# Kernel tuning notes

Hardware: AMD Instinct MI355X
Metric: run time of the kernel (lower is better)

Reference implementation:

```python
import jax, jax.numpy as jnp
import numpy as np
from jax import lax

B, L, D = 2, 1024, 1024
EXPAND, N, K = 2, 16, 4          # expand, d_state, d_conv
DI = EXPAND * D                  # d_inner = 2048
R = (D + 15) // 16               # dt_rank = 64
EPS = 1e-5


def setup_inputs() -> dict:
    key = jax.random.key(0)
    ks = jax.random.split(key, 8)
    x = jax.random.normal(ks[0], (B, L, D), dtype=jnp.float32)
    ln_w = jnp.ones((D,), jnp.float32)
    ln_b = jnp.zeros((D,), jnp.float32)
    W_in = jax.random.normal(ks[1], (D, 2 * DI), jnp.float32) * (1.0 / np.sqrt(D))
    conv_w = jax.random.normal(ks[2], (DI, K), jnp.float32) * 0.2
    conv_b = jnp.zeros((DI,), jnp.float32)
    W_x = jax.random.normal(ks[3], (DI, R + 2 * N), jnp.float32) * (1.0 / np.sqrt(DI))
    W_dt = jax.random.normal(ks[4], (R, DI), jnp.float32) * (1.0 / np.sqrt(R))
    b_dt = jnp.full((DI,), -4.0, jnp.float32)  # softplus(-4) ~ 0.018 dt init
    A_log = jnp.log(jnp.broadcast_to(jnp.arange(1, N + 1, dtype=jnp.float32), (DI, N)))
    D_param = jnp.ones((DI,), jnp.float32)
    W_out = jax.random.normal(ks[5], (DI, D), jnp.float32) * (1.0 / np.sqrt(DI))
    return {"x": x, "ln_w": ln_w, "ln_b": ln_b, "W_in": W_in, "conv_w": conv_w,
            "conv_b": conv_b, "W_x": W_x, "W_dt": W_dt, "b_dt": b_dt,
            "A_log": A_log, "D_param": D_param, "W_out": W_out}


def _mamba_block(x, ln_w, ln_b, W_in, conv_w, conv_b, W_x, W_dt, b_dt, A_log, D_param, W_out):
    # pre-LayerNorm
    mu = jnp.mean(x, axis=-1, keepdims=True)
    xc = x - mu
    var = jnp.mean(xc * xc, axis=-1, keepdims=True)
    h = xc * lax.rsqrt(var + EPS) * ln_w + ln_b          # [B,L,D]

    xz = h @ W_in                                        # [B,L,2*DI]
    xi, z = xz[..., :DI], xz[..., DI:]

    # depthwise causal conv1d, kernel K, left pad K-1
    xp = jnp.pad(xi, ((0, 0), (K - 1, 0), (0, 0)))
    conv = conv_b
    for k in range(K):
        conv = conv + xp[:, k:k + L, :] * conv_w[:, k]
    u = jax.nn.silu(conv)                                # [B,L,DI]

    proj = u @ W_x                                       # [B,L,R+2N]
    dt_r = proj[..., :R]
    Bm = proj[..., R:R + N]                              # [B,L,N]
    Cm = proj[..., R + N:]                               # [B,L,N]
    dt = jax.nn.softplus(dt_r @ W_dt + b_dt)             # [B,L,DI]

    A = -jnp.exp(A_log)                                  # [DI,N]
    dA = jnp.exp(dt[..., None] * A)                      # [B,L,DI,N]
    dBu = (dt * u)[..., None] * Bm[:, :, None, :]        # [B,L,DI,N]

    def comb(e1, e2):
        a1, b1 = e1
        a2, b2 = e2
        return a1 * a2, a2 * b1 + b2

    _, hs = lax.associative_scan(comb, (dA, dBu), axis=1)  # [B,L,DI,N]
    y = jnp.einsum('bldn,bln->bld', hs, Cm) + u * D_param
    y = y * jax.nn.silu(z)
    return x + y @ W_out


def reference(x, ln_w, ln_b, W_in, conv_w, conv_b, W_x, W_dt, b_dt, A_log, D_param, W_out):
    return _mamba_block(x, ln_w, ln_b, W_in, conv_w, conv_b, W_x, W_dt, b_dt,
                        A_log, D_param, W_out)
```

## Files before the change

### kernel.cpp

```cpp
#include <hip/hip_runtime.h>
#include <hip/hip_bf16.h>
#include <math.h>

#define B_ 2
#define L_ 1024
#define D_ 1024
#define DI_ 2048
#define K_ 4
#define N_ 16
#define R_ 64
#define BL_ (B_ * L_)
#define EPS_ 1e-5f

#define IDX4(l) ((l) + (((l) >> 6) << 2))

typedef __attribute__((ext_vector_type(8))) short short8;
typedef __attribute__((ext_vector_type(4))) float f32x4;

__device__ inline unsigned short f2bf(float f) {
    unsigned u = __float_as_uint(f);
    unsigned r = (u + 0x7fffu + ((u >> 16) & 1u)) >> 16;
    return (unsigned short)r;
}
__device__ inline float bf2f(unsigned short s) {
    return __uint_as_float(((unsigned)s) << 16);
}
__device__ inline float fast_silu(float z) {
    return z * __builtin_amdgcn_rcpf(1.f + __expf(-z));
}
__device__ inline void gl_lds16(const void* g, void* l) {
    __builtin_amdgcn_global_load_lds(
        (const __attribute__((address_space(1))) void*)g,
        (__attribute__((address_space(3))) void*)l, 16, 0, 0);
}

template <int CTRL>
__device__ inline float dpp_shr(float x) {
    return __int_as_float(__builtin_amdgcn_update_dpp(
        0, __float_as_int(x), CTRL, 0xf, 0xf, true));
}
__device__ inline float row16_sum(float p) {
    p += dpp_shr<0x111>(p);
    p += dpp_shr<0x112>(p);
    p += dpp_shr<0x114>(p);
    p += dpp_shr<0x118>(p);
    return p;
}

__global__ void ln_kernel(const float* __restrict__ x, const float* __restrict__ w,
                          const float* __restrict__ b, unsigned short* __restrict__ hb) {
    int row = blockIdx.x;
    const float* xr = x + (size_t)row * D_;
    float4 v = ((const float4*)xr)[threadIdx.x];

    __shared__ float red[4];
    float s = v.x + v.y + v.z + v.w;
    for (int off = 1; off < 64; off <<= 1) s += __shfl_xor(s, off, 64);
    if ((threadIdx.x & 63) == 0) red[threadIdx.x >> 6] = s;
    __syncthreads();
    float mu = (red[0] + red[1] + red[2] + red[3]) * (1.0f / D_);
    __syncthreads();
    float cx = v.x - mu, cy = v.y - mu, cz = v.z - mu, cw = v.w - mu;
    float sq = cx*cx + cy*cy + cz*cz + cw*cw;
    for (int off = 1; off < 64; off <<= 1) sq += __shfl_xor(sq, off, 64);
    if ((threadIdx.x & 63) == 0) red[threadIdx.x >> 6] = sq;
    __syncthreads();
    float var = (red[0] + red[1] + red[2] + red[3]) * (1.0f / D_);
    float rstd = rsqrtf(var + EPS_);

    float4 wv = ((const float4*)w)[threadIdx.x];
    float4 bv = ((const float4*)b)[threadIdx.x];
    ushort4 o;
    o.x = f2bf(cx * rstd * wv.x + bv.x);
    o.y = f2bf(cy * rstd * wv.y + bv.y);
    o.z = f2bf(cz * rstd * wv.z + bv.z);
    o.w = f2bf(cw * rstd * wv.w + bv.w);
    ((ushort4*)(hb + (size_t)row * D_))[threadIdx.x] = o;
}

__global__ void transpose_cast_all(const float* __restrict__ W_in, const float* __restrict__ W_x,
                                   const float* __restrict__ W_out,
                                   unsigned short* __restrict__ WinT, unsigned short* __restrict__ WxT,
                                   unsigned short* __restrict__ WoutT) {
    int bid = blockIdx.x;
    const float* W; unsigned short* WT; int K, N, bx, by;
    if (bid < 4096)      { W = W_in;  WT = WinT;  K = 1024; N = 4096; bx = bid & 127; by = bid >> 7; }
    else if (bid < 4288) { int id = bid - 4096; W = W_x;  WT = WxT;  K = DI_; N = 96;   bx = id % 3;  by = id / 3; }
    else                 { int id = bid - 4288; W = W_out; WT = WoutT; K = DI_; N = 1024; bx = id & 31; by = id >> 5; }
    __shared__ float tile[32][33];
    int k0 = by * 32, n0 = bx * 32;
    int tr = threadIdx.x >> 5;
    int tc = threadIdx.x & 31;
#pragma unroll
    for (int i = 0; i < 4; ++i)
        tile[tr + i*8][tc] = W[(size_t)(k0 + tr + i*8) * N + n0 + tc];
    __syncthreads();
#pragma unroll
    for (int i = 0; i < 4; ++i)
        WT[(size_t)(n0 + tr + i*8) * K + k0 + tc] = f2bf(tile[tc][tr + i*8]);
}

template <int BN, int MODE>
__global__ __launch_bounds__(256) void mfma_gemm_bt(
        const unsigned short* __restrict__ A,  int lda,
        const unsigned short* __restrict__ BT, int ldb,
        float* __restrict__ C, int ldc, int Kchunk,
        unsigned short* __restrict__ xi, unsigned short* __restrict__ sz) {
    constexpr int NT = BN / 32;
    __shared__ unsigned short As[128 * 32];
    __shared__ unsigned short Bs[BN * 32];

    int tid = threadIdx.x;
    int wave = tid >> 6, lane = tid & 63;
    int lane15 = lane & 15, quad = lane >> 4;
    int wr = wave >> 1, wc = wave & 1;

    int m0 = blockIdx.y * 128;
    int n0 = blockIdx.x * BN;
    int kbeg = blockIdx.z * Kchunk;
    int kend = kbeg + Kchunk;

    f32x4 acc[4][NT];
#pragma unroll
    for (int i = 0; i < 4; ++i)
#pragma unroll
        for (int j = 0; j < NT; ++j) acc[i][j] = (f32x4){0.f, 0.f, 0.f, 0.f};

    constexpr int ACALLS = 8;
    constexpr int BCALLS = BN * 4 / 64;

    for (int k0 = kbeg; k0 < kend; k0 += 32) {
        __syncthreads();
        for (int c = wave; c < ACALLS + BCALLS; c += 4) {
            if (c < ACALLS) {
                int cell = c * 64 + lane;
                int m = cell >> 2, s = cell & 3;
                int q = s ^ (m & 3) ^ ((m >> 2) & 3);
                gl_lds16(A + (size_t)(m0 + m) * lda + k0 + q * 8, &As[c * 512]);
            } else {
                int cell = (c - ACALLS) * 64 + lane;
                int n = cell >> 2, s = cell & 3;
                int q = s ^ (n & 3) ^ ((n >> 2) & 3);
                gl_lds16(BT + (size_t)(n0 + n) * ldb + k0 + q * 8, &Bs[(c - ACALLS) * 512]);
            }
        }
        __syncthreads();

        short8 af[4], bfr[NT];
#pragma unroll
        for (int i = 0; i < 4; ++i) {
            int m = wr * 64 + i * 16 + lane15;
            int s = quad ^ (m & 3) ^ ((m >> 2) & 3);
            af[i] = *(const short8*)&As[m * 32 + s * 8];
        }
#pragma unroll
        for (int j = 0; j < NT; ++j) {
            int n = wc * (NT * 16) + j * 16 + lane15;
            int s = quad ^ (n & 3) ^ ((n >> 2) & 3);
            bfr[j] = *(const short8*)&Bs[n * 32 + s * 8];
        }
#pragma unroll
        for (int i = 0; i < 4; ++i)
#pragma unroll
            for (int j = 0; j < NT; ++j)
                acc[i][j] = __builtin_amdgcn_mfma_f32_16x16x32_bf16(af[i], bfr[j], acc[i][j], 0, 0, 0);
    }

#pragma unroll
    for (int i = 0; i < 4; ++i) {
        int row = m0 + wr * 64 + i * 16 + quad * 4;
#pragma unroll
        for (int j = 0; j < NT; ++j) {
            int col = n0 + wc * (NT * 16) + j * 16 + lane15;
#pragma unroll
            for (int r = 0; r < 4; ++r) {
                float v = acc[i][j][r];
                int rr = row + r;
                if (MODE == 0) {
                    C[(size_t)rr * ldc + col] = v;
                } else if (MODE == 1) {
                    atomicAdd(&C[(size_t)rr * ldc + col], v);
                } else {
                    if (col < DI_) xi[(size_t)rr * DI_ + col] = f2bf(v);
                    else           sz[(size_t)rr * DI_ + (col - DI_)] = f2bf(fast_silu(v));
                }
            }
        }
    }
}

__global__ void conv_silu_kernel(const unsigned short* __restrict__ xi, const float* __restrict__ cw,
                                 const float* __restrict__ cb, unsigned short* __restrict__ ub) {
    int idx = blockIdx.x * blockDim.x + threadIdx.x;
    int c4 = (idx << 2) & (DI_ - 1);
    int bl = (idx << 2) >> 11;
    int l = bl & (L_ - 1);
    float4 w0 = ((const float4*)cw)[c4 + 0];
    float4 w1 = ((const float4*)cw)[c4 + 1];
    float4 w2 = ((const float4*)cw)[c4 + 2];
    float4 w3 = ((const float4*)cw)[c4 + 3];
    float4 cbv = *(const float4*)&cb[c4];
    float a0 = cbv.x, a1 = cbv.y, a2 = cbv.z, a3 = cbv.w;
    const unsigned short* base = xi + (size_t)bl * DI_ + c4;

    ushort4 t0 = *(const ushort4*)base;
    a0 = fmaf(bf2f(t0.x), w0.w, a0); a1 = fmaf(bf2f(t0.y), w1.w, a1);
    a2 = fmaf(bf2f(t0.z), w2.w, a2); a3 = fmaf(bf2f(t0.w), w3.w, a3);
    if (l >= 1) {
        ushort4 t1 = *(const ushort4*)(base - DI_);
        a0 = fmaf(bf2f(t1.x), w0.z, a0); a1 = fmaf(bf2f(t1.y), w1.z, a1);
        a2 = fmaf(bf2f(t1.z), w2.z, a2); a3 = fmaf(bf2f(t1.w), w3.z, a3);
    }
    if (l >= 2) {
        ushort4 t2 = *(const ushort4*)(base - 2 * DI_);
        a0 = fmaf(bf2f(t2.x), w0.y, a0); a1 = fmaf(bf2f(t2.y), w1.y, a1);
        a2 = fmaf(bf2f(t2.z), w2.y, a2); a3 = fmaf(bf2f(t2.w), w3.y, a3);
    }
    if (l >= 3) {
        ushort4 t3 = *(const ushort4*)(base - 3 * DI_);
        a0 = fmaf(bf2f(t3.x), w0.x, a0); a1 = fmaf(bf2f(t3.y), w1.x, a1);
        a2 = fmaf(bf2f(t3.z), w2.x, a2); a3 = fmaf(bf2f(t3.w), w3.x, a3);
    }
    ushort4 o;
    o.x = f2bf(fast_silu(a0)); o.y = f2bf(fast_silu(a1));
    o.z = f2bf(fast_silu(a2)); o.w = f2bf(fast_silu(a3));
    *(ushort4*)(ub + (size_t)bl * DI_ + c4) = o;
}

__global__ __launch_bounds__(256) void dtprep(
        const float* __restrict__ proj, const float* __restrict__ W_dt,
        const float* __restrict__ b_dt, const unsigned short* __restrict__ ub,
        const unsigned short* __restrict__ szb, const float* __restrict__ Dp,
        float2* __restrict__ dtduT, unsigned int* __restrict__ szdT) {
    __shared__ alignas(16) unsigned char smem[64 * 65 * 8];
    float (*As)[68] = reinterpret_cast<float(*)[68]>(smem);
    float (*Bs)[64] = reinterpret_cast<float(*)[64]>(smem + 4352);
    float2 (*T2)[65] = reinterpret_cast<float2(*)[65]>(smem);
    unsigned int (*TU)[65] = reinterpret_cast<unsigned int(*)[65]>(smem);

    int tid = threadIdx.x;
    int n0 = blockIdx.x * 64;
    int m0 = blockIdx.y * 64;
    int ar = tid >> 2, ak = (tid & 3) << 2;
    int kb = tid >> 4, bc = (tid & 15) << 2;
    int ty = tid >> 4, tx = tid & 15;

    float acc[4][4] = {};
#pragma unroll
    for (int k0 = 0; k0 < R_; k0 += 16) {
        float4 av = *(const float4*)&proj[(size_t)(m0 + ar) * 96 + k0 + ak];
        As[ak + 0][ar] = av.x; As[ak + 1][ar] = av.y;
        As[ak + 2][ar] = av.z; As[ak + 3][ar] = av.w;
        float4 bv = *(const float4*)&W_dt[(size_t)(k0 + kb) * DI_ + n0 + bc];
        Bs[kb][bc + 0] = bv.x; Bs[kb][bc + 1] = bv.y;
        Bs[kb][bc + 2] = bv.z; Bs[kb][bc + 3] = bv.w;
        __syncthreads();
#pragma unroll
        for (int kk = 0; kk < 16; ++kk) {
            float a[4], bb[4];
#pragma unroll
            for (int i = 0; i < 4; ++i) a[i] = As[kk][ty * 4 + i];
#pragma unroll
            for (int j = 0; j < 4; ++j) bb[j] = Bs[kk][tx * 4 + j];
#pragma unroll
            for (int i = 0; i < 4; ++i)
#pragma unroll
                for (int j = 0; j < 4; ++j)
                    acc[i][j] = fmaf(a[i], bb[j], acc[i][j]);
        }
        __syncthreads();
    }

    float4 bd = *(const float4*)&b_dt[n0 + tx * 4];
    float4 dp4 = *(const float4*)&Dp[n0 + tx * 4];
    float bda[4] = {bd.x, bd.y, bd.z, bd.w};
    float dpa[4] = {dp4.x, dp4.y, dp4.z, dp4.w};
    float2 d2[4][4];
    unsigned int su[4][4];
#pragma unroll
    for (int i = 0; i < 4; ++i) {
        int bl = m0 + ty * 4 + i;
        ushort4 u4 = *(const ushort4*)&ub[(size_t)bl * DI_ + n0 + tx * 4];
        ushort4 s4 = *(const ushort4*)&szb[(size_t)bl * DI_ + n0 + tx * 4];
        unsigned short ua[4] = {u4.x, u4.y, u4.z, u4.w};
        unsigned short sa[4] = {s4.x, s4.y, s4.z, s4.w};
#pragma unroll
        for (int j = 0; j < 4; ++j) {
            float v = acc[i][j] + bda[j];
            float dtv = fmaxf(v, 0.f) + __logf(1.f + __expf(-fabsf(v)));
            float uu = bf2f(ua[j]);
            float szv = bf2f(sa[j]);
            d2[i][j] = make_float2(dtv, dtv * uu);
            su[i][j] = ((unsigned)f2bf(uu * dpa[j] * szv) << 16) | (unsigned)f2bf(szv);
        }
    }

#pragma unroll
    for (int i = 0; i < 4; ++i)
#pragma unroll
        for (int j = 0; j < 4; ++j)
            T2[ty * 4 + i][tx * 4 + j] = d2[i][j];
    __syncthreads();
#pragma unroll
    for (int i = 0; i < 8; ++i) {
        int c_l = (tid >> 5) + i * 8;
#pragma unroll
        for (int jj = 0; jj < 2; ++jj) {
            int bl_l = (tid & 31) + jj * 32;
            dtduT[(size_t)(n0 + c_l) * BL_ + m0 + bl_l] = T2[bl_l][c_l];
        }
    }
    __syncthreads();

#pragma unroll
    for (int i = 0; i < 4; ++i)
#pragma unroll
        for (int j = 0; j < 4; ++j)
            TU[ty * 4 + i][tx * 4 + j] = su[i][j];
    __syncthreads();
#pragma unroll
    for (int i = 0; i < 8; ++i) {
        int c_l = (tid >> 5) + i * 8;
#pragma unroll
        for (int jj = 0; jj < 2; ++jj) {
            int bl_l = (tid & 31) + jj * 32;
            szdT[(size_t)(n0 + c_l) * BL_ + m0 + bl_l] = TU[bl_l][c_l];
        }
    }
}

__global__ __launch_bounds__(256) void scan_v5(
        const float2* __restrict__ dtduT, const unsigned int* __restrict__ szdT,
        const float* __restrict__ proj, const float* __restrict__ A_log,
        unsigned short* __restrict__ yzT) {
    int bc = blockIdx.x;
    int b = bc >> 10;
    int cp = bc & 1023;
    int t = threadIdx.x;
    int n = t & 15;
    int cs = (t >> 4) & 1;
    int chunk = t >> 5;
    int c = cp * 2 + cs;

    __shared__ float dd[2][(L_ + 32) * 2];
    __shared__ float sA[8][32];
    __shared__ float sB[8][32];
    __shared__ float ps[2][L_ + 64];

    {
        int half = t >> 7;
        int tt = t & 127;
        int l = tt * 8;
        int cload = cp * 2 + half;
        const float4* g = (const float4*)(dtduT + (size_t)cload * BL_ + (size_t)b * L_ + l);
        int il2 = l + ((l >> 6) << 1);
        float* dst = &dd[half][il2 * 2];
        *(float4*)(dst + 0)  = g[0];
        *(float4*)(dst + 4)  = g[1];
        *(float4*)(dst + 8)  = g[2];
        *(float4*)(dst + 12) = g[3];
    }
    __syncthreads();

    float A = -__expf(A_log[c * N_ + n]);
    int l0 = chunk * 128;
    const float* pB = proj + (size_t)b * L_ * 96 + R_ + n;
    const float* pC = pB + N_;

    float a = 1.f, acc = 0.f;
#pragma unroll
    for (int h = 0; h < 2; ++h) {
        int lb = l0 + h * 64;
        const float* ddp = &dd[cs][(lb + ((lb >> 6) << 1)) * 2];
        const float* pBb = pB + (size_t)lb * 96;
#pragma unroll
        for (int q = 0; q < 16; ++q) {
            float4 d0 = *(const float4*)(ddp + q * 8);
            float4 d1 = *(const float4*)(ddp + q * 8 + 4);
            float b0 = pBb[(q*4 + 0) * 96];
            float b1 = pBb[(q*4 + 1) * 96];
            float b2 = pBb[(q*4 + 2) * 96];
            float b3 = pBb[(q*4 + 3) * 96];
            float e;
            e = __expf(d0.x * A); a *= e; acc = fmaf(e, acc, d0.y * b0);
            e = __expf(d0.z * A); a *= e; acc = fmaf(e, acc, d0.w * b1);
            e = __expf(d1.x * A); a *= e; acc = fmaf(e, acc, d1.y * b2);
            e = __expf(d1.z * A); a *= e; acc = fmaf(e, acc, d1.w * b3);
        }
    }
    sA[chunk][t & 31] = a;
    sB[chunk][t & 31] = acc;
    __syncthreads();

    if (t < 32) {
        float hc = 0.f;
#pragma unroll
        for (int j = 0; j < 8; ++j) {
            float aj = sA[j][t];
            float bj = sB[j][t];
            sB[j][t] = hc;
            hc = fmaf(aj, hc, bj);
        }
    }
    __syncthreads();
    float h = sB[chunk][t & 31];

#pragma unroll
    for (int hh = 0; hh < 2; ++hh) {
        int lb = l0 + hh * 64;
        const float* ddp = &dd[cs][(lb + ((lb >> 6) << 1)) * 2];
        const float* pBb = pB + (size_t)lb * 96;
        const float* pCb = pC + (size_t)lb * 96;
        float* psb = &ps[cs][IDX4(lb)];
#pragma unroll
        for (int q = 0; q < 16; ++q) {
            float4 d0 = *(const float4*)(ddp + q * 8);
            float4 d1 = *(const float4*)(ddp + q * 8 + 4);
            float b0 = pBb[(q*4 + 0) * 96], c0 = pCb[(q*4 + 0) * 96];
            float b1 = pBb[(q*4 + 1) * 96], c1 = pCb[(q*4 + 1) * 96];
            float b2 = pBb[(q*4 + 2) * 96], c2 = pCb[(q*4 + 2) * 96];
            float b3 = pBb[(q*4 + 3) * 96], c3 = pCb[(q*4 + 3) * 96];
            float e, p0, p1, p2, p3;
            e = __expf(d0.x * A); h = fmaf(e, h, d0.y * b0); p0 = row16_sum(h * c0);
            e = __expf(d0.z * A); h = fmaf(e, h, d0.w * b1); p1 = row16_sum(h * c1);
            e = __expf(d1.x * A); h = fmaf(e, h, d1.y * b2); p2 = row16_sum(h * c2);
            e = __expf(d1.z * A); h = fmaf(e, h, d1.w * b3); p3 = row16_sum(h * c3);
            if (n == 15) *(float4*)&psb[q * 4] = (float4){p0, p1, p2, p3};
        }
    }
    __syncthreads();

    {
        int half = t >> 7;
        int tt = t & 127;
        int l = tt * 8;
        int c_out = cp * 2 + half;
        size_t tb = (size_t)c_out * BL_ + (size_t)b * L_;
        const float* pp = &ps[half][IDX4(l)];
        ushort4 o[2];
#pragma unroll
        for (int g = 0; g < 2; ++g) {
            float4 p4 = *(const float4*)(pp + g * 4);
            uint4 sd4 = *(const uint4*)(szdT + tb + l + g * 4);
            o[g].x = f2bf(p4.x * bf2f((unsigned short)(sd4.x & 0xffff)) + bf2f((unsigned short)(sd4.x >> 16)));
            o[g].y = f2bf(p4.y * bf2f((unsigned short)(sd4.y & 0xffff)) + bf2f((unsigned short)(sd4.y >> 16)));
            o[g].z = f2bf(p4.z * bf2f((unsigned short)(sd4.z & 0xffff)) + bf2f((unsigned short)(sd4.z >> 16)));
            o[g].w = f2bf(p4.w * bf2f((unsigned short)(sd4.w & 0xffff)) + bf2f((unsigned short)(sd4.w >> 16)));
        }
        *(ushort4*)(yzT + tb + l) = o[0];
        *(ushort4*)(yzT + tb + l + 4) = o[1];
    }
}

__global__ void transpose_y(const unsigned short* __restrict__ yzT, unsigned short* __restrict__ yz) {
    __shared__ unsigned short t[32][33];
    int c0 = blockIdx.y * 32, bl0 = blockIdx.x * 32;
    int r = threadIdx.x >> 5;
    int col = threadIdx.x & 31;
#pragma unroll
    for (int i = 0; i < 4; ++i)
        t[r + i*8][col] = yzT[(size_t)(c0 + r + i*8) * BL_ + bl0 + col];
    __syncthreads();
#pragma unroll
    for (int i = 0; i < 4; ++i)
        yz[(size_t)(bl0 + r + i*8) * DI_ + c0 + col] = t[col][r + i*8];
}

extern "C" void kernel_launch(void* const* d_in, const int* in_sizes, int n_in,
                              void* d_out, int out_size, void* d_ws, size_t ws_size,
                              hipStream_t stream) {
    const float* x       = (const float*)d_in[0];
    const float* ln_w    = (const float*)d_in[1];
    const float* ln_b    = (const float*)d_in[2];
    const float* W_in    = (const float*)d_in[3];
    const float* conv_w  = (const float*)d_in[4];
    const float* conv_b  = (const float*)d_in[5];
    const float* W_x     = (const float*)d_in[6];
    const float* W_dt    = (const float*)d_in[7];
    const float* b_dt    = (const float*)d_in[8];
    const float* A_log   = (const float*)d_in[9];
    const float* D_param = (const float*)d_in[10];
    const float* W_out   = (const float*)d_in[11];
    float* out = (float*)d_out;

    uint8_t* p = (uint8_t*)d_ws;
    unsigned short* hb    = (unsigned short*)p;  p += (size_t)BL_ * D_ * 2;
    unsigned short* WinT  = (unsigned short*)p;  p += (size_t)4096 * 1024 * 2;
    unsigned short* xib   = (unsigned short*)p;  p += (size_t)BL_ * DI_ * 2;
    unsigned short* szb   = (unsigned short*)p;  p += (size_t)BL_ * DI_ * 2;
    unsigned short* ub    = (unsigned short*)p;  p += (size_t)BL_ * DI_ * 2;
    unsigned short* WxT   = (unsigned short*)p;  p += (size_t)96 * DI_ * 2;
    float*          proj  = (float*)p;           p += (size_t)BL_ * 96 * 4;
    unsigned short* WoutT = (unsigned short*)p;  p += (size_t)1024 * DI_ * 2;
    float2*         dtduT = (float2*)p;          p += (size_t)BL_ * DI_ * 8;
    unsigned int*   szdT  = (unsigned int*)p;    p += (size_t)BL_ * DI_ * 4;
    unsigned short* yzT   = (unsigned short*)p;  p += (size_t)BL_ * DI_ * 2;
    unsigned short* yzb   = (unsigned short*)d_ws;

    hipMemsetAsync(proj, 0, (size_t)BL_ * 96 * 4, stream);
    hipMemcpyAsync(out, x, (size_t)BL_ * D_ * 4, hipMemcpyDeviceToDevice, stream);

    transpose_cast_all<<<6336, 256, 0, stream>>>(W_in, W_x, W_out, WinT, WxT, WoutT);

    ln_kernel<<<BL_, 256, 0, stream>>>(x, ln_w, ln_b, hb);

    mfma_gemm_bt<128, 3><<<dim3(4096 / 128, BL_ / 128, 1), 256, 0, stream>>>(
        hb, 1024, WinT, 1024, nullptr, 0, 1024, xib, szb);

    conv_silu_kernel<<<(BL_ * DI_) / 1024, 256, 0, stream>>>(xib, conv_w, conv_b, ub);

    mfma_gemm_bt<96, 1><<<dim3(1, BL_ / 128, 16), 256, 0, stream>>>(
        ub, DI_, WxT, DI_, proj, 96, 128, nullptr, nullptr);

    dtprep<<<dim3(DI_ / 64, BL_ / 64), 256, 0, stream>>>(
        proj, W_dt, b_dt, ub, szb, D_param, dtduT, szdT);

    scan_v5<<<B_ * DI_ / 2, 256, 0, stream>>>(dtduT, szdT, proj, A_log, yzT);

    transpose_y<<<dim3(BL_ / 32, DI_ / 32), 256, 0, stream>>>(yzT, yzb);

    mfma_gemm_bt<128, 1><<<dim3(1024 / 128, BL_ / 128, 2), 256, 0, stream>>>(
        yzb, DI_, WoutT, DI_, out, 1024, 1024, nullptr, nullptr);
}
```

Measured before the change: 292.3 us.

## Pack dt/du as bf16 pairs, move gating into transpose, merge prologue kernels

dtprep now writes one packed 32-bit word per element, holding bf16 dt and bf16 dt*u, instead of a float2 plus a separate skip/gate word. That shrinks both the intermediate dtprep writes and the scan reads, and removes one transposed stream. The D skip term and the silu(z) gate move from the scan into the transpose kernel, which reads u and sz directly in row-major order. The weight transpose, LayerNorm, residual copy and proj zeroing are merged into a single prologue launch. Storing dt in bf16 loses some precision in the exp(dt*A) term.

Result: no change. 289.4 us (-1.0%).

```diff
diff --git a/kernel.cpp b/kernel.cpp
--- a/kernel.cpp
+++ b/kernel.cpp
@@ -47,57 +47,69 @@
     return p;
 }
 
-__global__ void ln_kernel(const float* __restrict__ x, const float* __restrict__ w,
-                          const float* __restrict__ b, unsigned short* __restrict__ hb) {
-    int row = blockIdx.x;
-    const float* xr = x + (size_t)row * D_;
-    float4 v = ((const float4*)xr)[threadIdx.x];
-
+__global__ void prologue(const float* __restrict__ W_in, const float* __restrict__ W_x,
+                         const float* __restrict__ W_out, const float* __restrict__ x,
+                         const float* __restrict__ lnw, const float* __restrict__ lnb,
+                         unsigned short* __restrict__ WinT, unsigned short* __restrict__ WxT,
+                         unsigned short* __restrict__ WoutT, unsigned short* __restrict__ hb,
+                         float* __restrict__ out, float* __restrict__ proj) {
+    __shared__ float tile[32][33];
     __shared__ float red[4];
-    float s = v.x + v.y + v.z + v.w;
-    for (int off = 1; off < 64; off <<= 1) s += __shfl_xor(s, off, 64);
-    if ((threadIdx.x & 63) == 0) red[threadIdx.x >> 6] = s;
-    __syncthreads();
-    float mu = (red[0] + red[1] + red[2] + red[3]) * (1.0f / D_);
-    __syncthreads();
-    float cx = v.x - mu, cy = v.y - mu, cz = v.z - mu, cw = v.w - mu;
-    float sq = cx*cx + cy*cy + cz*cz + cw*cw;
-    for (int off = 1; off < 64; off <<= 1) sq += __shfl_xor(sq, off, 64);
-    if ((threadIdx.x & 63) == 0) red[threadIdx.x >> 6] = sq;
-    __syncthreads();
-    float var = (red[0] + red[1] + red[2] + red[3]) * (1.0f / D_);
-    float rstd = rsqrtf(var + EPS_);
-
-    float4 wv = ((const float4*)w)[threadIdx.x];
-    float4 bv = ((const float4*)b)[threadIdx.x];
-    ushort4 o;
-    o.x = f2bf(cx * rstd * wv.x + bv.x);
-    o.y = f2bf(cy * rstd * wv.y + bv.y);
-    o.z = f2bf(cz * rstd * wv.z + bv.z);
-    o.w = f2bf(cw * rstd * wv.w + bv.w);
-    ((ushort4*)(hb + (size_t)row * D_))[threadIdx.x] = o;
-}
-
-__global__ void transpose_cast_all(const float* __restrict__ W_in, const float* __restrict__ W_x,
-                                   const float* __restrict__ W_out,
-                                   unsigned short* __restrict__ WinT, unsigned short* __restrict__ WxT,
-                                   unsigned short* __restrict__ WoutT) {
     int bid = blockIdx.x;
-    const float* W; unsigned short* WT; int K, N, bx, by;
-    if (bid < 4096)      { W = W_in;  WT = WinT;  K = 1024; N = 4096; bx = bid & 127; by = bid >> 7; }
-    else if (bid < 4288) { int id = bid - 4096; W = W_x;  WT = WxT;  K = DI_; N = 96;   bx = id % 3;  by = id / 3; }
-    else                 { int id = bid - 4288; W = W_out; WT = WoutT; K = DI_; N = 1024; bx = id & 31; by = id >> 5; }
-    __shared__ float tile[32][33];
-    int k0 = by * 32, n0 = bx * 32;
-    int tr = threadIdx.x >> 5;
-    int tc = threadIdx.x & 31;
-#pragma unroll
-    for (int i = 0; i < 4; ++i)
-        tile[tr + i*8][tc] = W[(size_t)(k0 + tr + i*8) * N + n0 + tc];
-    __syncthreads();
-#pragma unroll
-    for (int i = 0; i < 4; ++i)
-        WT[(size_t)(n0 + tr + i*8) * K + k0 + tc] = f2bf(tile[tc][tr + i*8]);
+    int tid = threadIdx.x;
+
+    if (bid < 6336) {
+        const float* W; unsigned short* WT; int Kd, Nd, bx, by;
+        if (bid < 4096)      { W = W_in;  WT = WinT;  Kd = 1024; Nd = 4096; bx = bid & 127; by = bid >> 7; }
+        else if (bid < 4288) { int id = bid - 4096; W = W_x;  WT = WxT;  Kd = DI_; Nd = 96;   bx = id % 3;  by = id / 3; }
+        else                 { int id = bid - 4288; W = W_out; WT = WoutT; Kd = DI_; Nd = 1024; bx = id & 31; by = id >> 5; }
+        int k0 = by * 32, n0 = bx * 32;
+        int tr = tid >> 5, tc = tid & 31;
+#pragma unroll
+        for (int i = 0; i < 4; ++i)
+            tile[tr + i*8][tc] = W[(size_t)(k0 + tr + i*8) * Nd + n0 + tc];
+        __syncthreads();
+#pragma unroll
+        for (int i = 0; i < 4; ++i)
+            WT[(size_t)(n0 + tr + i*8) * Kd + k0 + tc] = f2bf(tile[tc][tr + i*8]);
+    } else if (bid < 8384) {
+        int row = bid - 6336;
+        const float* xr = x + (size_t)row * D_;
+        float4 v = ((const float4*)xr)[tid];
+        float s = v.x + v.y + v.z + v.w;
+        for (int off = 1; off < 64; off <<= 1) s += __shfl_xor(s, off, 64);
+        if ((tid & 63) == 0) red[tid >> 6] = s;
+        __syncthreads();
+        float mu = (red[0] + red[1] + red[2] + red[3]) * (1.0f / D_);
+        __syncthreads();
+        float cx = v.x - mu, cy = v.y - mu, cz = v.z - mu, cw = v.w - mu;
+        float sq = cx*cx + cy*cy + cz*cz + cw*cw;
+        for (int off = 1; off < 64; off <<= 1) sq += __shfl_xor(sq, off, 64);
+        if ((tid & 63) == 0) red[tid >> 6] = sq;
+        __syncthreads();
+        float var = (red[0] + red[1] + red[2] + red[3]) * (1.0f / D_);
+        float rstd = rsqrtf(var + EPS_);
+        float4 wv = ((const float4*)lnw)[tid];
+        float4 bv = ((const float4*)lnb)[tid];
+        ushort4 o;
+        o.x = f2bf(cx * rstd * wv.x + bv.x);
+        o.y = f2bf(cy * rstd * wv.y + bv.y);
+        o.z = f2bf(cz * rstd * wv.z + bv.z);
+        o.w = f2bf(cw * rstd * wv.w + bv.w);
+        ((ushort4*)(hb + (size_t)row * D_))[tid] = o;
+    } else if (bid < 8896) {
+        int base = (bid - 8384) * 1024;
+#pragma unroll
+        for (int i = 0; i < 4; ++i) {
+            int idx = base + i * 256 + tid;
+            ((float4*)out)[idx] = ((const float4*)x)[idx];
+        }
+    } else {
+        int base = (bid - 8896) * 1024;
+#pragma unroll
+        for (int i = 0; i < 4; ++i)
+            ((float4*)proj)[base + i * 256 + tid] = (float4){0.f, 0.f, 0.f, 0.f};
+    }
 }
 
 template <int BN, int MODE>
@@ -230,12 +242,10 @@
 __global__ __launch_bounds__(256) void dtprep(
         const float* __restrict__ proj, const float* __restrict__ W_dt,
         const float* __restrict__ b_dt, const unsigned short* __restrict__ ub,
-        const unsigned short* __restrict__ szb, const float* __restrict__ Dp,
-        float2* __restrict__ dtduT, unsigned int* __restrict__ szdT) {
-    __shared__ alignas(16) unsigned char smem[64 * 65 * 8];
+        unsigned int* __restrict__ dtduT) {
+    __shared__ alignas(16) unsigned char smem[64 * 65 * 4];
     float (*As)[68] = reinterpret_cast<float(*)[68]>(smem);
     float (*Bs)[64] = reinterpret_cast<float(*)[64]>(smem + 4352);
-    float2 (*T2)[65] = reinterpret_cast<float2(*)[65]>(smem);
     unsigned int (*TU)[65] = reinterpret_cast<unsigned int(*)[65]>(smem);
 
     int tid = threadIdx.x;
@@ -272,45 +282,21 @@
     }
 
     float4 bd = *(const float4*)&b_dt[n0 + tx * 4];
-    float4 dp4 = *(const float4*)&Dp[n0 + tx * 4];
     float bda[4] = {bd.x, bd.y, bd.z, bd.w};
-    float dpa[4] = {dp4.x, dp4.y, dp4.z, dp4.w};
-    float2 d2[4][4];
     unsigned int su[4][4];
 #pragma unroll
     for (int i = 0; i < 4; ++i) {
         int bl = m0 + ty * 4 + i;
         ushort4 u4 = *(const ushort4*)&ub[(size_t)bl * DI_ + n0 + tx * 4];
-        ushort4 s4 = *(const ushort4*)&szb[(size_t)bl * DI_ + n0 + tx * 4];
         unsigned short ua[4] = {u4.x, u4.y, u4.z, u4.w};
-        unsigned short sa[4] = {s4.x, s4.y, s4.z, s4.w};
 #pragma unroll
         for (int j = 0; j < 4; ++j) {
             float v = acc[i][j] + bda[j];
             float dtv = fmaxf(v, 0.f) + __logf(1.f + __expf(-fabsf(v)));
-            float uu = bf2f(ua[j]);
-            float szv = bf2f(sa[j]);
-            d2[i][j] = make_float2(dtv, dtv * uu);
-            su[i][j] = ((unsigned)f2bf(uu * dpa[j] * szv) << 16) | (unsigned)f2bf(szv);
-        }
-    }
-
-#pragma unroll
-    for (int i = 0; i < 4; ++i)
-#pragma unroll
-        for (int j = 0; j < 4; ++j)
-            T2[ty * 4 + i][tx * 4 + j] = d2[i][j];
-    __syncthreads();
-#pragma unroll
-    for (int i = 0; i < 8; ++i) {
-        int c_l = (tid >> 5) + i * 8;
-#pragma unroll
-        for (int jj = 0; jj < 2; ++jj) {
-            int bl_l = (tid & 31) + jj * 32;
-            dtduT[(size_t)(n0 + c_l) * BL_ + m0 + bl_l] = T2[bl_l][c_l];
-        }
-    }
-    __syncthreads();
+            float du = dtv * bf2f(ua[j]);
+            su[i][j] = ((unsigned)f2bf(dtv) << 16) | (unsigned)f2bf(du);
+        }
+    }
 
 #pragma unroll
     for (int i = 0; i < 4; ++i)
@@ -324,15 +310,14 @@
 #pragma unroll
         for (int jj = 0; jj < 2; ++jj) {
             int bl_l = (tid & 31) + jj * 32;
-            szdT[(size_t)(n0 + c_l) * BL_ + m0 + bl_l] = TU[bl_l][c_l];
-        }
-    }
-}
-
-__global__ __launch_bounds__(256) void scan_v5(
-        const float2* __restrict__ dtduT, const unsigned int* __restrict__ szdT,
-        const float* __restrict__ proj, const float* __restrict__ A_log,
-        unsigned short* __restrict__ yzT) {
+            dtduT[(size_t)(n0 + c_l) * BL_ + m0 + bl_l] = TU[bl_l][c_l];
+        }
+    }
+}
+
+__global__ __launch_bounds__(256) void scan_v9(
+        const unsigned int* __restrict__ dtduT, const float* __restrict__ proj,
+        const float* __restrict__ A_log, unsigned short* __restrict__ yzT) {
     int bc = blockIdx.x;
     int b = bc >> 10;
     int cp = bc & 1023;
@@ -342,7 +327,7 @@
     int chunk = t >> 5;
     int c = cp * 2 + cs;
 
-    __shared__ float dd[2][(L_ + 32) * 2];
+    __shared__ unsigned int dd[2][L_ + 32];
     __shared__ float sA[8][32];
     __shared__ float sB[8][32];
     __shared__ float ps[2][L_ + 64];
@@ -351,14 +336,10 @@
         int half = t >> 7;
         int tt = t & 127;
         int l = tt * 8;
-        int cload = cp * 2 + half;
-        const float4* g = (const float4*)(dtduT + (size_t)cload * BL_ + (size_t)b * L_ + l);
-        int il2 = l + ((l >> 6) << 1);
-        float* dst = &dd[half][il2 * 2];
-        *(float4*)(dst + 0)  = g[0];
-        *(float4*)(dst + 4)  = g[1];
-        *(float4*)(dst + 8)  = g[2];
-        *(float4*)(dst + 12) = g[3];
+        const uint4* g = (const uint4*)(dtduT + (size_t)(cp * 2 + half) * BL_ + (size_t)b * L_ + l);
+        int il = l + ((l >> 6) << 1);
+        *(uint4*)&dd[half][il]     = g[0];
+        *(uint4*)&dd[half][il + 4] = g[1];
     }
     __syncthreads();
 
@@ -371,21 +352,20 @@
 #pragma unroll
     for (int h = 0; h < 2; ++h) {
         int lb = l0 + h * 64;
-        const float* ddp = &dd[cs][(lb + ((lb >> 6) << 1)) * 2];
+        const unsigned int* ddp = &dd[cs][lb + ((lb >> 6) << 1)];
         const float* pBb = pB + (size_t)lb * 96;
 #pragma unroll
         for (int q = 0; q < 16; ++q) {
-            float4 d0 = *(const float4*)(ddp + q * 8);
-            float4 d1 = *(const float4*)(ddp + q * 8 + 4);
+            uint4 u4 = *(const uint4*)(ddp + q * 4);
             float b0 = pBb[(q*4 + 0) * 96];
             float b1 = pBb[(q*4 + 1) * 96];
             float b2 = pBb[(q*4 + 2) * 96];
             float b3 = pBb[(q*4 + 3) * 96];
             float e;
-            e = __expf(d0.x * A); a *= e; acc = fmaf(e, acc, d0.y * b0);
-            e = __expf(d0.z * A); a *= e; acc = fmaf(e, acc, d0.w * b1);
-            e = __expf(d1.x * A); a *= e; acc = fmaf(e, acc, d1.y * b2);
-            e = __expf(d1.z * A); a *= e; acc = fmaf(e, acc, d1.w * b3);
+            e = __expf(__uint_as_float(u4.x & 0xffff0000u) * A); a *= e; acc = fmaf(e, acc, __uint_as_float(u4.x << 16) * b0);
+            e = __expf(__uint_as_float(u4.y & 0xffff0000u) * A); a *= e; acc = fmaf(e, acc, __uint_as_float(u4.y << 16) * b1);
+            e = __expf(__uint_as_float(u4.z & 0xffff0000u) * A); a *= e; acc = fmaf(e, acc, __uint_as_float(u4.z << 16) * b2);
+            e = __expf(__uint_as_float(u4.w & 0xffff0000u) * A); a *= e; acc = fmaf(e, acc, __uint_as_float(u4.w << 16) * b3);
         }
     }
     sA[chunk][t & 31] = a;
@@ -408,23 +388,22 @@
 #pragma unroll
     for (int hh = 0; hh < 2; ++hh) {
         int lb = l0 + hh * 64;
-        const float* ddp = &dd[cs][(lb + ((lb >> 6) << 1)) * 2];
+        const unsigned int* ddp = &dd[cs][lb + ((lb >> 6) << 1)];
         const float* pBb = pB + (size_t)lb * 96;
         const float* pCb = pC + (size_t)lb * 96;
         float* psb = &ps[cs][IDX4(lb)];
 #pragma unroll
         for (int q = 0; q < 16; ++q) {
-            float4 d0 = *(const float4*)(ddp + q * 8);
-            float4 d1 = *(const float4*)(ddp + q * 8 + 4);
+            uint4 u4 = *(const uint4*)(ddp + q * 4);
             float b0 = pBb[(q*4 + 0) * 96], c0 = pCb[(q*4 + 0) * 96];
             float b1 = pBb[(q*4 + 1) * 96], c1 = pCb[(q*4 + 1) * 96];
             float b2 = pBb[(q*4 + 2) * 96], c2 = pCb[(q*4 + 2) * 96];
             float b3 = pBb[(q*4 + 3) * 96], c3 = pCb[(q*4 + 3) * 96];
             float e, p0, p1, p2, p3;
-            e = __expf(d0.x * A); h = fmaf(e, h, d0.y * b0); p0 = row16_sum(h * c0);
-            e = __expf(d0.z * A); h = fmaf(e, h, d0.w * b1); p1 = row16_sum(h * c1);
-            e = __expf(d1.x * A); h = fmaf(e, h, d1.y * b2); p2 = row16_sum(h * c2);
-            e = __expf(d1.z * A); h = fmaf(e, h, d1.w * b3); p3 = row16_sum(h * c3);
+            e = __expf(__uint_as_float(u4.x & 0xffff0000u) * A); h = fmaf(e, h, __uint_as_float(u4.x << 16) * b0); p0 = row16_sum(h * c0);
+            e = __expf(__uint_as_float(u4.y & 0xffff0000u) * A); h = fmaf(e, h, __uint_as_float(u4.y << 16) * b1); p1 = row16_sum(h * c1);
+            e = __expf(__uint_as_float(u4.z & 0xffff0000u) * A); h = fmaf(e, h, __uint_as_float(u4.z << 16) * b2); p2 = row16_sum(h * c2);
+            e = __expf(__uint_as_float(u4.w & 0xffff0000u) * A); h = fmaf(e, h, __uint_as_float(u4.w << 16) * b3); p3 = row16_sum(h * c3);
             if (n == 15) *(float4*)&psb[q * 4] = (float4){p0, p1, p2, p3};
         }
     }
@@ -437,22 +416,19 @@
         int c_out = cp * 2 + half;
         size_t tb = (size_t)c_out * BL_ + (size_t)b * L_;
         const float* pp = &ps[half][IDX4(l)];
-        ushort4 o[2];
-#pragma unroll
-        for (int g = 0; g < 2; ++g) {
-            float4 p4 = *(const float4*)(pp + g * 4);
-            uint4 sd4 = *(const uint4*)(szdT + tb + l + g * 4);
-            o[g].x = f2bf(p4.x * bf2f((unsigned short)(sd4.x & 0xffff)) + bf2f((unsigned short)(sd4.x >> 16)));
-            o[g].y = f2bf(p4.y * bf2f((unsigned short)(sd4.y & 0xffff)) + bf2f((unsigned short)(sd4.y >> 16)));
-            o[g].z = f2bf(p4.z * bf2f((unsigned short)(sd4.z & 0xffff)) + bf2f((unsigned short)(sd4.z >> 16)));
-            o[g].w = f2bf(p4.w * bf2f((unsigned short)(sd4.w & 0xffff)) + bf2f((unsigned short)(sd4.w >> 16)));
-        }
-        *(ushort4*)(yzT + tb + l) = o[0];
-        *(ushort4*)(yzT + tb + l + 4) = o[1];
-    }
-}
-
-__global__ void transpose_y(const unsigned short* __restrict__ yzT, unsigned short* __restrict__ yz) {
+        ushort4 o0, o1;
+        o0.x = f2bf(pp[0]); o0.y = f2bf(pp[1]); o0.z = f2bf(pp[2]); o0.w = f2bf(pp[3]);
+        o1.x = f2bf(pp[4]); o1.y = f2bf(pp[5]); o1.z = f2bf(pp[6]); o1.w = f2bf(pp[7]);
+        *(ushort4*)(yzT + tb + l) = o0;
+        *(ushort4*)(yzT + tb + l + 4) = o1;
+    }
+}
+
+__global__ void transpose_gate(const unsigned short* __restrict__ yzT,
+                               const unsigned short* __restrict__ ub,
+                               const unsigned short* __restrict__ szb,
+                               const float* __restrict__ Dp,
+                               unsigned short* __restrict__ yz) {
     __shared__ unsigned short t[32][33];
     int c0 = blockIdx.y * 32, bl0 = blockIdx.x * 32;
     int r = threadIdx.x >> 5;
@@ -461,9 +437,17 @@
     for (int i = 0; i < 4; ++i)
         t[r + i*8][col] = yzT[(size_t)(c0 + r + i*8) * BL_ + bl0 + col];
     __syncthreads();
-#pragma unroll
-    for (int i = 0; i < 4; ++i)
-        yz[(size_t)(bl0 + r + i*8) * DI_ + c0 + col] = t[col][r + i*8];
+    int c = c0 + col;
+    float Dv = Dp[c];
+#pragma unroll
+    for (int i = 0; i < 4; ++i) {
+        int bl = bl0 + r + i*8;
+        size_t off = (size_t)bl * DI_ + c;
+        float p = bf2f(t[col][r + i*8]);
+        float uu = bf2f(ub[off]);
+        float sz = bf2f(szb[off]);
+        yz[off] = f2bf((p + uu * Dv) * sz);
+    }
 }
 
 extern "C" void kernel_launch(void* const* d_in, const int* in_sizes, int n_in,
@@ -492,17 +476,12 @@
     unsigned short* WxT   = (unsigned short*)p;  p += (size_t)96 * DI_ * 2;
     float*          proj  = (float*)p;           p += (size_t)BL_ * 96 * 4;
     unsigned short* WoutT = (unsigned short*)p;  p += (size_t)1024 * DI_ * 2;
-    float2*         dtduT = (float2*)p;          p += (size_t)BL_ * DI_ * 8;
-    unsigned int*   szdT  = (unsigned int*)p;    p += (size_t)BL_ * DI_ * 4;
+    unsigned int*   dtduT = (unsigned int*)p;    p += (size_t)BL_ * DI_ * 4;
     unsigned short* yzT   = (unsigned short*)p;  p += (size_t)BL_ * DI_ * 2;
     unsigned short* yzb   = (unsigned short*)d_ws;
 
-    hipMemsetAsync(proj, 0, (size_t)BL_ * 96 * 4, stream);
-    hipMemcpyAsync(out, x, (size_t)BL_ * D_ * 4, hipMemcpyDeviceToDevice, stream);
-
-    transpose_cast_all<<<6336, 256, 0, stream>>>(W_in, W_x, W_out, WinT, WxT, WoutT);
-
-    ln_kernel<<<BL_, 256, 0, stream>>>(x, ln_w, ln_b, hb);
+    prologue<<<8944, 256, 0, stream>>>(W_in, W_x, W_out, x, ln_w, ln_b,
+                                       WinT, WxT, WoutT, hb, out, proj);
 
     mfma_gemm_bt<128, 3><<<dim3(4096 / 128, BL_ / 128, 1), 256, 0, stream>>>(
         hb, 1024, WinT, 1024, nullptr, 0, 1024, xib, szb);
@@ -513,11 +492,11 @@
         ub, DI_, WxT, DI_, proj, 96, 128, nullptr, nullptr);
 
     dtprep<<<dim3(DI_ / 64, BL_ / 64), 256, 0, stream>>>(
-        proj, W_dt, b_dt, ub, szb, D_param, dtduT, szdT);
-
-    scan_v5<<<B_ * DI_ / 2, 256, 0, stream>>>(dtduT, szdT, proj, A_log, yzT);
-
-    transpose_y<<<dim3(BL_ / 32, DI_ / 32), 256, 0, stream>>>(yzT, yzb);
+        proj, W_dt, b_dt, ub, dtduT);
+
+    scan_v9<<<B_ * DI_ / 2, 256, 0, stream>>>(dtduT, proj, A_log, yzT);
+
+    transpose_gate<<<dim3(BL_ / 32, DI_ / 32), 256, 0, stream>>>(yzT, ub, szb, D_param, yzb);
 
     mfma_gemm_bt<128, 1><<<dim3(1024 / 128, BL_ / 128, 2), 256, 0, stream>>>(
         yzb, DI_, WoutT, DI_, out, 1024, 1024, nullptr, nullptr);
```
